# Kernel optimization log

Hardware: AMD Instinct MI355X
Metric: run time of the kernel (lower is better)

## Reference

```python
import jax, jax.numpy as jnp
from jax import lax
import numpy as np


def _gru_step(gi, h, Whh, bhh):
    # torch GRU cell: gates ordered (r, z, n); gi = x @ Wih.T + bih precomputed
    gh = h @ Whh.T + bhh
    ir, iz, inn = jnp.split(gi, 3, axis=-1)
    hr, hz, hn = jnp.split(gh, 3, axis=-1)
    r = jax.nn.sigmoid(ir + hr)
    z = jax.nn.sigmoid(iz + hz)
    n = jnp.tanh(inn + r * hn)
    return (1.0 - z) * n + z * h


def setup_inputs() -> dict:
    key = jax.random.key(0)
    ks = jax.random.split(key, 12)
    B, T, F, Wd, H, L = 64, 80, 4096, 6000, 512, 32
    s = 0.05  # weight init scale
    return {
        "x": jax.random.uniform(ks[0], (B, T, F), jnp.float32),  # nonneg CNN features -> full video lengths
        "y": jax.random.randint(ks[1], (L, B), 0, Wd),           # time-major caption token ids
        "Wih_v": jax.random.normal(ks[2], (3 * H, F), jnp.float32) * s,
        "Whh_v": jax.random.normal(ks[3], (3 * H, H), jnp.float32) * s,
        "bih_v": jax.random.normal(ks[4], (3 * H,), jnp.float32) * s,
        "bhh_v": jax.random.normal(ks[5], (3 * H,), jnp.float32) * s,
        "Wih_c": jax.random.normal(ks[6], (3 * H, H + Wd), jnp.float32) * s,
        "Whh_c": jax.random.normal(ks[7], (3 * H, H), jnp.float32) * s,
        "bih_c": jax.random.normal(ks[8], (3 * H,), jnp.float32) * s,
        "bhh_c": jax.random.normal(ks[9], (3 * H,), jnp.float32) * s,
        "Wout": jax.random.normal(ks[10], (Wd, H), jnp.float32) * s,
        "bout": jax.random.normal(ks[11], (Wd,), jnp.float32) * s,
    }


def reference(x, y, Wih_v, Whh_v, bih_v, bhh_v, Wih_c, Whh_c, bih_c, bhh_c, Wout, bout):
    B, T, F = x.shape
    L = y.shape[0]
    H = Whh_v.shape[1]
    Wd = Wout.shape[0]
    dt = x.dtype

    # ---- encode stage: video GRU over full-length sequences (time-major) ----
    xs = jnp.transpose(x, (1, 0, 2))                       # [T,B,F]
    gi_v = jnp.einsum('tbf,gf->tbg', xs, Wih_v) + bih_v    # precompute input gates
    h0 = jnp.zeros((B, H), dt)

    def enc_v(h, gi):
        h2 = _gru_step(gi, h, Whh_v, bhh_v)
        return h2, h2

    _, enc_out = lax.scan(enc_v, h0, gi_v)                 # [T,B,H]

    # caption GRU over [enc_out ; zeros(word_dim)]; zero word part contributes nothing
    Wih_c_h = Wih_c[:, :H]                                 # [3H,H]
    Wih_c_w = Wih_c[:, H:]                                 # [3H,Wd]
    gi_c = jnp.einsum('tbh,gh->tbg', enc_out, Wih_c_h) + bih_c

    def enc_c(h, gi):
        h2 = _gru_step(gi, h, Whh_c, bhh_c)
        return h2, None

    # NOTE: original code assigns this final hidden to `hidden_video` (quirk preserved)
    hidden_video, _ = lax.scan(enc_c, h0, gi_c)            # [B,H]

    # ---- decode stage: steps i = 1 .. L-1, zero frame input, teacher forcing ----
    gi_zero = jnp.broadcast_to(bih_v, (B, 3 * H))          # x=0 -> input gates are just bias
    WcwT = Wih_c_w.T                                       # [Wd,3H]; one-hot matmul == row gather

    def dec(h_v, y_prev):
        h_v2 = _gru_step(gi_zero, h_v, Whh_v, bhh_v)
        gi = h_v2 @ Wih_c_h.T + WcwT[y_prev] + bih_c       # concat([out, one_hot(y_prev)]) @ Wih_c.T
        h_c = _gru_step(gi, h_v2, Whh_c, bhh_c)            # initial hidden = fresh video hidden (original quirk)
        logits = h_c @ Wout.T + bout
        return h_v2, logits

    _, logits = lax.scan(dec, hidden_video, y[:-1])        # [L-1,B,Wd]

    probs = jnp.zeros((B, L, Wd), dt)
    probs = probs.at[0, 0, 1].set(1.0)                     # probs[0,:,1]=1 survives only at t=0
    probs = probs.at[:, 1:].set(jnp.transpose(logits, (1, 0, 2)))

    # loss is overwritten each iteration in the original -> last step only (cross-entropy)
    logp = jax.nn.log_softmax(logits[-1], axis=-1)         # [B,Wd]
    loss = -jnp.take_along_axis(logp, y[-1][:, None], axis=1).mean()
    return probs, loss
```

## Files before the change

kernel.cpp:

```cpp
#include <hip/hip_runtime.h>

typedef short s16x8 __attribute__((ext_vector_type(8)));
typedef float f32x4 __attribute__((ext_vector_type(4)));
typedef unsigned short u16x4 __attribute__((ext_vector_type(4)));

#define MFMA_B16(a, b, c) __builtin_amdgcn_mfma_f32_16x16x32_bf16((a), (b), (c), 0, 0, 0)

__device__ __forceinline__ unsigned short f2b(float f) {
    unsigned u = __builtin_bit_cast(unsigned, f);
    u = (u + 0x7fffu + ((u >> 16) & 1u)) >> 16;
    return (unsigned short)u;
}
__device__ __forceinline__ float b2f(unsigned short h) {
    unsigned u = ((unsigned)h) << 16;
    return __builtin_bit_cast(float, u);
}
__device__ __forceinline__ float sigm(float x) { return 1.f / (1.f + __expf(-x)); }
__device__ __forceinline__ float tanh_f(float x) {
    float t = __expf(-2.f * fabsf(x));
    float r = (1.f - t) / (1.f + t);
    return copysignf(r, x);
}

__device__ __forceinline__ void stg_b16_sc(unsigned short* p, unsigned short v) {
    unsigned v32 = v;
    asm volatile("global_store_short %0, %1, off sc1" :: "v"(p), "v"(v32) : "memory");
}
__device__ __forceinline__ void stg_b32_sc(float* p, float v) {
    asm volatile("global_store_dword %0, %1, off sc1" :: "v"(p), "v"(v) : "memory");
}
__device__ __forceinline__ unsigned long long ldg_u64_sc(const void* p) {
    return __hip_atomic_load((unsigned long long*)p, __ATOMIC_RELAXED, __HIP_MEMORY_SCOPE_AGENT);
}
__device__ __forceinline__ float ldg_b16_sc(const unsigned short* p) {
    unsigned short v = __hip_atomic_load((unsigned short*)p, __ATOMIC_RELAXED, __HIP_MEMORY_SCOPE_AGENT);
    return b2f(v);
}
__device__ __forceinline__ float ldg_f32_sc(const float* p) {
    return __hip_atomic_load((float*)p, __ATOMIC_RELAXED, __HIP_MEMORY_SCOPE_AGENT);
}
__device__ __forceinline__ s16x8 ldA_sc(const unsigned short* p) {
    union { unsigned long long u[2]; s16x8 v; } r;
    r.u[0] = ldg_u64_sc(p);
    r.u[1] = ldg_u64_sc((const unsigned long long*)p + 1);
    return r.v;
}

__device__ __forceinline__ void block_publish(int* flag, int v) {
    asm volatile("s_waitcnt vmcnt(0)" ::: "memory");
    __syncthreads();
    if (threadIdx.x == 0)
        __hip_atomic_store(flag, v, __ATOMIC_RELAXED, __HIP_MEMORY_SCOPE_AGENT);
}
template <int SLP>
__device__ __forceinline__ void flags_wait2(const int* f1, int t1, const int* f2, int t2) {
    const int lane = threadIdx.x & 63;
    const int* ptr = (lane < 32) ? (f1 + lane * 16) : (f2 + (lane - 32) * 16);
    const int tgt = (lane < 32) ? t1 : t2;
    for (;;) {
        int v = __hip_atomic_load((int*)ptr, __ATOMIC_RELAXED, __HIP_MEMORY_SCOPE_AGENT);
        if (__all(v >= tgt)) break;
        __builtin_amdgcn_s_sleep(SLP);
    }
}
template <int SLP>
__device__ __forceinline__ void flags_wait(const int* f, int t) {
    flags_wait2<SLP>(f, t, f, t);
}
template <int SLP>
__device__ __forceinline__ void scalar_wait(int* c, int target) {
    while (__hip_atomic_load(c, __ATOMIC_RELAXED, __HIP_MEMORY_SCOPE_AGENT) < target)
        __builtin_amdgcn_s_sleep(SLP);
}
__device__ __forceinline__ void wave_add(int* c) {
    asm volatile("s_waitcnt vmcnt(0)" ::: "memory");
    if ((threadIdx.x & 63) == 0)
        __hip_atomic_fetch_add(c, 1, __ATOMIC_RELAXED, __HIP_MEMORY_SCOPE_AGENT);
}

#define WTILE 8192
#define WF(Wl, t, c, lane) (*(const s16x8*)((Wl) + (((t) * 16 + (c)) * 64 + (lane)) * 8))

__device__ __forceinline__ void stage_swz(const unsigned short* __restrict__ src,
                                          unsigned short* dst) {
    for (int idx = threadIdx.x; idx < 1024; idx += 256) {
        const int ln = idx & 63;
        *(uint4*)(dst + (size_t)idx * 8) =
            *(const uint4*)(src + (size_t)(ln & 15) * 512 + (ln >> 4) * 8 + ((idx >> 6)) * 32);
    }
}

__device__ __forceinline__ void mm3_s(const unsigned short* __restrict__ A, int m0,
                                      const unsigned short* Wl, int lane,
                                      f32x4& a0, f32x4& a1, f32x4& a2) {
    const unsigned short* ab = A + (size_t)(m0 + (lane & 15)) * 512 + (lane >> 4) * 8;
#pragma unroll
    for (int c = 0; c < 16; ++c) {
        s16x8 a = ldA_sc(ab + c * 32);
        a0 = MFMA_B16(a, WF(Wl, 0, c, lane), a0);
        a1 = MFMA_B16(a, WF(Wl, 1, c, lane), a1);
        a2 = MFMA_B16(a, WF(Wl, 2, c, lane), a2);
    }
}
__device__ __forceinline__ void mm6_s(const unsigned short* __restrict__ A0,
                                      const unsigned short* __restrict__ A1, int m0,
                                      const unsigned short* Wl, int lane,
                                      f32x4& aR, f32x4& aZ, f32x4& aIN, f32x4& aHN) {
    const unsigned short* a0 = A0 + (size_t)(m0 + (lane & 15)) * 512 + (lane >> 4) * 8;
    const unsigned short* a1 = A1 + (size_t)(m0 + (lane & 15)) * 512 + (lane >> 4) * 8;
#pragma unroll
    for (int c = 0; c < 16; ++c) {
        s16x8 x0 = ldA_sc(a0 + c * 32);
        s16x8 x1 = ldA_sc(a1 + c * 32);
        aR  = MFMA_B16(x0, WF(Wl, 0, c, lane), aR);
        aZ  = MFMA_B16(x0, WF(Wl, 1, c, lane), aZ);
        aIN = MFMA_B16(x0, WF(Wl, 2, c, lane), aIN);
        aR  = MFMA_B16(x1, WF(Wl, 3, c, lane), aR);
        aZ  = MFMA_B16(x1, WF(Wl, 4, c, lane), aZ);
        aHN = MFMA_B16(x1, WF(Wl, 5, c, lane), aHN);
    }
}

__global__ void prep_kernel(const float* __restrict__ x, const float* __restrict__ Wih_v,
                            const float* __restrict__ Whh_v, const float* __restrict__ Whh_c,
                            const float* __restrict__ Wih_c, const float* __restrict__ Wout,
                            unsigned short* __restrict__ xB, unsigned short* __restrict__ WihB,
                            unsigned short* __restrict__ WhhvB, unsigned short* __restrict__ WhhcB,
                            unsigned short* __restrict__ WchhB, unsigned short* __restrict__ WoutB,
                            unsigned short* __restrict__ zeroB, int* __restrict__ ctrs,
                            float* __restrict__ out) {
    const int n = gridDim.x * blockDim.x;
    const int id0 = blockIdx.x * blockDim.x + threadIdx.x;
    for (int i = id0; i < 5242880; i += n) {
        const int e = i * 4;
        const int f = e & 4095, bt = e >> 12;
        const int b = bt / 80, t = bt - b * 80;
        float4 v = *(const float4*)(x + (size_t)e);
        u16x4 s = {f2b(v.x), f2b(v.y), f2b(v.z), f2b(v.w)};
        *(u16x4*)(xB + (size_t)(t * 64 + b) * 4096 + f) = s;
    }
    for (int i = id0; i < 1572864; i += n) {
        float4 v = *(const float4*)(Wih_v + (size_t)i * 4);
        u16x4 s = {f2b(v.x), f2b(v.y), f2b(v.z), f2b(v.w)};
        *(u16x4*)(WihB + (size_t)i * 4) = s;
    }
    for (int i = id0; i < 786432; i += n) {
        WhhvB[i] = f2b(Whh_v[i]);
        WhhcB[i] = f2b(Whh_c[i]);
        WchhB[i] = f2b(Wih_c[(size_t)(i >> 9) * 6512 + (i & 511)]);
    }
    for (int i = id0; i < 3072000; i += n) WoutB[i] = f2b(Wout[i]);
    for (int i = id0; i < 384000; i += n)
        out[(size_t)(i / 6000) * 192000 + (i % 6000)] = (i == 1) ? 1.f : 0.f;
    for (int i = id0; i < 32768; i += n) zeroB[i] = 0;
    for (int i = id0; i < 4096; i += n) ctrs[i] = 0;
}

__global__ __launch_bounds__(256) void gemm1_kernel(const unsigned short* __restrict__ xB,
                                                    const unsigned short* __restrict__ WihB,
                                                    const float* __restrict__ bih,
                                                    float* __restrict__ gi) {
    __shared__ unsigned short As[128 * 40];
    __shared__ unsigned short Bs[128 * 40];
    const int bm = blockIdx.x % 40;
    const int bn = blockIdx.x / 40;
    const int m0 = bm * 128, n0 = bn * 128;
    const int tid = threadIdx.x;
    const int lane = tid & 63;
    const int wave = tid >> 6;
    const int wm = (wave >> 1) * 64, wn = (wave & 1) * 64;
    const int quad = lane >> 4, l15 = lane & 15;

    const f32x4 z4 = {0.f, 0.f, 0.f, 0.f};
    f32x4 acc[4][4];
#pragma unroll
    for (int i = 0; i < 4; ++i)
#pragma unroll
        for (int j = 0; j < 4; ++j) acc[i][j] = z4;

    const int sr = tid >> 1;
    const int sc0 = (tid & 1) * 16;

    for (int k0 = 0; k0 < 4096; k0 += 32) {
        __syncthreads();
#pragma unroll
        for (int p = 0; p < 2; ++p) {
            const int c8 = sc0 + p * 8;
            *(s16x8*)&As[sr * 40 + c8] =
                *(const s16x8*)(xB + (size_t)(m0 + sr) * 4096 + k0 + c8);
            *(s16x8*)&Bs[sr * 40 + c8] =
                *(const s16x8*)(WihB + (size_t)(n0 + sr) * 4096 + k0 + c8);
        }
        __syncthreads();
        s16x8 af[4], bfr[4];
#pragma unroll
        for (int i = 0; i < 4; ++i) af[i] = *(const s16x8*)&As[(wm + i * 16 + l15) * 40 + quad * 8];
#pragma unroll
        for (int j = 0; j < 4; ++j) bfr[j] = *(const s16x8*)&Bs[(wn + j * 16 + l15) * 40 + quad * 8];
#pragma unroll
        for (int i = 0; i < 4; ++i)
#pragma unroll
            for (int j = 0; j < 4; ++j) acc[i][j] = MFMA_B16(af[i], bfr[j], acc[i][j]);
    }
#pragma unroll
    for (int i = 0; i < 4; ++i)
#pragma unroll
        for (int j = 0; j < 4; ++j)
#pragma unroll
            for (int r = 0; r < 4; ++r) {
                const int m = m0 + wm + i * 16 + quad * 4 + r;
                const int nn = n0 + wn + j * 16 + l15;
                gi[(size_t)m * 1536 + nn] = acc[i][j][r] + bih[nn];
            }
}

struct SeqParams {
    const float* bih_v; const float* bhh_v;
    const float* bih_c; const float* bhh_c;
    const float* bout;  const int* y;
    const float* gi;    const float* Wc;  float* out;
    const unsigned short* WhhvB; const unsigned short* WhhcB; const unsigned short* WchhB;
    const unsigned short* WoutB; unsigned short* WcwTB;
    unsigned short* eo;
    unsigned short* hv2B;
    float*          hv2F;
    unsigned short* hcdB;
    unsigned short* ecb0; unsigned short* ecb1; unsigned short* zeroB;
    float* hcf; float* lossP; int* ctr;
};
#define F_EO (p.ctr)
#define F_EC (p.ctr + 512)
#define F_HV (p.ctr + 1024)
#define F_HC (p.ctr + 1536)
#define S_TR (p.ctr + 2048)
#define S_LOG (p.ctr + 2064)
#define S_LP (p.ctr + 2080)

__global__ __launch_bounds__(256, 1) void seq_kernel(SeqParams p) {
    __shared__ unsigned short Wlds[49152];
    const int blk = blockIdx.x;
    const int lane = threadIdx.x & 63;
    const int wave = threadIdx.x >> 6;
    const int quad = lane >> 4, l15 = lane & 15;
    const f32x4 z4 = {0.f, 0.f, 0.f, 0.f};

    if (blk < 32) {
        const int j0 = blk * 16;
        const int j = j0 + l15;
        const int m0 = wave * 16;
        const int b_ = m0 + quad * 4;
#pragma unroll
        for (int g = 0; g < 3; ++g)
            stage_swz(p.WhhvB + (size_t)(g * 512 + j0) * 512, Wlds + g * WTILE);
        __syncthreads();
        const float bhr = p.bhh_v[j], bhz = p.bhh_v[512 + j], bhn = p.bhh_v[1024 + j];
        float hp[4] = {0.f, 0.f, 0.f, 0.f};

        for (int t = 0; t < 80; ++t) {
            float gr[4], gz[4], gn[4];
            const float* gt = p.gi + (size_t)t * 98304;
#pragma unroll
            for (int r = 0; r < 4; ++r) {
                const float* gb = gt + (size_t)(b_ + r) * 1536;
                gr[r] = gb[j]; gz[r] = gb[512 + j]; gn[r] = gb[1024 + j];
            }
            f32x4 aR = z4, aZ = z4, aN = z4;
            if (t > 0) {
                flags_wait<1>(F_EO, t);
                mm3_s(p.eo + (size_t)(t - 1) * 32768, m0, Wlds, lane, aR, aZ, aN);
            }
            unsigned short* eoW = p.eo + (size_t)t * 32768;
#pragma unroll
            for (int r = 0; r < 4; ++r) {
                float rg = sigm(gr[r] + aR[r] + bhr);
                float zg = sigm(gz[r] + aZ[r] + bhz);
                float ng = tanh_f(gn[r] + rg * (aN[r] + bhn));
                float hn = (1.f - zg) * ng + zg * hp[r];
                hp[r] = hn;
                stg_b16_sc(eoW + (size_t)(b_ + r) * 512 + j, f2b(hn));
            }
            block_publish(F_EO + blk * 16, t + 1);
        }

        flags_wait<1>(F_EC, 80);
        const float bir = p.bih_v[j], biz = p.bih_v[512 + j], bin_ = p.bih_v[1024 + j];
        for (int s = 0; s <= 30; ++s) {
            if (s > 0) flags_wait<1>(F_HV, s);
            f32x4 aR = z4, aZ = z4, aN = z4;
            mm3_s(p.hv2B + (size_t)s * 32768, m0, Wlds, lane, aR, aZ, aN);
            unsigned short* hw = p.hv2B + (size_t)(s + 1) * 32768;
            float* hwF = p.hv2F + (size_t)(s + 1) * 32768;
#pragma unroll
            for (int r = 0; r < 4; ++r) {
                float hpv = (s == 0) ? ldg_f32_sc(p.hcf + (size_t)(b_ + r) * 512 + j) : hp[r];
                float rg = sigm(bir + aR[r] + bhr);
                float zg = sigm(biz + aZ[r] + bhz);
                float ng = tanh_f(bin_ + rg * (aN[r] + bhn));
                float hn = (1.f - zg) * ng + zg * hpv;
                hp[r] = hn;
                stg_b16_sc(hw + (size_t)(b_ + r) * 512 + j, f2b(hn));
                stg_b32_sc(hwF + (size_t)(b_ + r) * 512 + j, hn);
            }
            block_publish(F_HV + blk * 16, s + 1);
        }

        if (blk < 16) {
            const int b = (blk << 2) | wave;
            scalar_wait<2>(S_LOG, 125);
            const float* lg = p.out + (size_t)b * 192000 + 186000;
            float m = -1e30f, sum = 0.f;
            for (int i = lane; i < 3000; i += 64) {
                union { unsigned long long u; float f[2]; } pr;
                pr.u = ldg_u64_sc(lg + 2 * i);
#pragma unroll
                for (int e = 0; e < 2; ++e) {
                    float v = pr.f[e];
                    float nm = fmaxf(m, v);
                    sum = sum * __expf(m - nm) + __expf(v - nm);
                    m = nm;
                }
            }
#pragma unroll
            for (int off = 32; off > 0; off >>= 1) {
                float m2 = __shfl_down(m, off);
                float s2 = __shfl_down(sum, off);
                float nm = fmaxf(m, m2);
                sum = sum * __expf(m - nm) + s2 * __expf(m2 - nm);
                m = nm;
            }
            if (lane == 0) {
                int yv = p.y[31 * 64 + b];
                float lgy = ldg_f32_sc(lg + yv);
                stg_b32_sc(p.lossP + b, (m + __logf(sum)) - lgy);
            }
            wave_add(S_LP);
            if (blk == 0 && wave == 0) {
                scalar_wait<1>(S_LP, 64);
                float v = ldg_f32_sc(p.lossP + lane);
#pragma unroll
                for (int off = 32; off > 0; off >>= 1) v += __shfl_down(v, off);
                if (lane == 0) p.out[12288000] = v * (1.f / 64.f);
            }
        }
    } else if (blk < 64) {
        const int cid = blk - 32;
        const int j0 = cid * 16;
        const int j = j0 + l15;
        const int m0 = wave * 16;
        const int b_ = m0 + quad * 4;
#pragma unroll
        for (int g = 0; g < 3; ++g) {
            stage_swz(p.WchhB + (size_t)(g * 512 + j0) * 512, Wlds + g * WTILE);
            stage_swz(p.WhhcB + (size_t)(g * 512 + j0) * 512, Wlds + (3 + g) * WTILE);
        }
        __syncthreads();
        const float bcr = p.bih_c[j] + p.bhh_c[j];
        const float bcz = p.bih_c[512 + j] + p.bhh_c[512 + j];
        const float bin_ = p.bih_c[1024 + j];
        const float bhn = p.bhh_c[1024 + j];
        float hp[4] = {0.f, 0.f, 0.f, 0.f};

        for (int t = 0; t < 80; ++t) {
            flags_wait2<1>(F_EO, t + 1, F_EC, t);
            const unsigned short* A1 = (t == 0) ? p.zeroB : ((t & 1) ? p.ecb0 : p.ecb1);
            unsigned short* ew = (t & 1) ? p.ecb1 : p.ecb0;
            f32x4 aR = z4, aZ = z4, aIN = z4, aHN = z4;
            mm6_s(p.eo + (size_t)t * 32768, A1, m0, Wlds, lane, aR, aZ, aIN, aHN);
#pragma unroll
            for (int r = 0; r < 4; ++r) {
                float rg = sigm(aR[r] + bcr);
                float zg = sigm(aZ[r] + bcz);
                float ng = tanh_f(aIN[r] + bin_ + rg * (aHN[r] + bhn));
                float hn = (1.f - zg) * ng + zg * hp[r];
                hp[r] = hn;
                unsigned short hb = f2b(hn);
                stg_b16_sc(ew + (size_t)(b_ + r) * 512 + j, hb);
                if (t == 79) {
                    stg_b16_sc(p.hv2B + (size_t)(b_ + r) * 512 + j, hb);
                    stg_b32_sc(p.hcf + (size_t)(b_ + r) * 512 + j, hn);
                }
            }
            block_publish(F_EC + cid * 16, t + 1);
        }

        scalar_wait<4>(S_TR, 94);
        for (int s = 0; s <= 30; ++s) {
            float er[4], ez[4], en[4];
#pragma unroll
            for (int r = 0; r < 4; ++r) {
                const int yv = p.y[s * 64 + (b_ + r)];
                const unsigned short* em = p.WcwTB + (size_t)yv * 1536;
                er[r] = ldg_b16_sc(em + j);
                ez[r] = ldg_b16_sc(em + 512 + j);
                en[r] = ldg_b16_sc(em + 1024 + j);
            }
            flags_wait<1>(F_HV, s + 1);
            const unsigned short* hv = p.hv2B + (size_t)(s + 1) * 32768;
            const float* hvF = p.hv2F + (size_t)(s + 1) * 32768;
            f32x4 aR = z4, aZ = z4, aIN = z4, aHN = z4;
            mm6_s(hv, hv, m0, Wlds, lane, aR, aZ, aIN, aHN);
            unsigned short* hc = p.hcdB + (size_t)s * 32768;
#pragma unroll
            for (int r = 0; r < 4; ++r) {
                float rg = sigm(aR[r] + er[r] + bcr);
                float zg = sigm(aZ[r] + ez[r] + bcz);
                float ng = tanh_f(aIN[r] + en[r] + bin_ + rg * (aHN[r] + bhn));
                float hpv = ldg_f32_sc(hvF + (size_t)(b_ + r) * 512 + j);
                stg_b16_sc(hc + (size_t)(b_ + r) * 512 + j, f2b((1.f - zg) * ng + zg * hpv));
            }
            block_publish(F_HC + cid * 16, s + 1);
        }
    } else {
        const int bo = blk - 64;
        const int w0 = bo * 48;
#pragma unroll
        for (int tl = 0; tl < 3; ++tl)
            stage_swz(p.WoutB + (size_t)(w0 + tl * 16) * 512, Wlds + tl * WTILE);
        __syncthreads();

        if (bo < 94) {
            float* tile = (float*)(Wlds + 24576);
            const int w0t = bo * 64;
            const int tx = threadIdx.x & 63, ty = threadIdx.x >> 6;
            for (int gt = 0; gt < 24; ++gt) {
                const int g0 = gt * 64;
                __syncthreads();
                for (int r = ty; r < 64; r += 4) {
                    int w = w0t + tx;
                    tile[r * 65 + tx] = (w < 6000) ? p.Wc[(size_t)(g0 + r) * 6512 + 512 + w] : 0.f;
                }
                __syncthreads();
                for (int r = ty; r < 64; r += 4) {
                    int w = w0t + r;
                    if (w < 6000)
                        stg_b16_sc(p.WcwTB + (size_t)w * 1536 + g0 + tx, f2b(tile[tx * 65 + r]));
                }
            }
            asm volatile("s_waitcnt vmcnt(0)" ::: "memory");
            __syncthreads();
            if (threadIdx.x == 0)
                __hip_atomic_fetch_add(S_TR, 1, __ATOMIC_RELAXED, __HIP_MEMORY_SCOPE_AGENT);
        }

        const int m0 = wave * 16;
        const int b_ = m0 + quad * 4;
        float bo_[3];
#pragma unroll
        for (int tl = 0; tl < 3; ++tl) bo_[tl] = p.bout[w0 + tl * 16 + l15];

        for (int s = 0; s <= 30; ++s) {
            flags_wait<2>(F_HC, s + 1);
            const unsigned short* ab =
                p.hcdB + (size_t)s * 32768 + (size_t)(m0 + l15) * 512 + quad * 8;
            s16x8 af[16];
#pragma unroll
            for (int c = 0; c < 16; ++c) af[c] = ldA_sc(ab + c * 32);
#pragma unroll
            for (int tl = 0; tl < 3; ++tl) {
                f32x4 acc = z4;
#pragma unroll
                for (int c = 0; c < 16; ++c) acc = MFMA_B16(af[c], WF(Wlds, tl, c, lane), acc);
#pragma unroll
                for (int r = 0; r < 4; ++r)
                    stg_b32_sc(p.out + (size_t)(b_ + r) * 192000 + (size_t)(s + 1) * 6000 +
                                   w0 + tl * 16 + l15,
                               acc[r] + bo_[tl]);
            }
        }
        asm volatile("s_waitcnt vmcnt(0)" ::: "memory");
        __syncthreads();
        if (threadIdx.x == 0)
            __hip_atomic_fetch_add(S_LOG, 1, __ATOMIC_RELAXED, __HIP_MEMORY_SCOPE_AGENT);
    }
}

extern "C" void kernel_launch(void* const* d_in, const int* in_sizes, int n_in,
                              void* d_out, int out_size, void* d_ws, size_t ws_size,
                              hipStream_t stream) {
    const float* x     = (const float*)d_in[0];
    const int*   y     = (const int*)d_in[1];
    const float* Wih_v = (const float*)d_in[2];
    const float* Whh_v = (const float*)d_in[3];
    const float* bih_v = (const float*)d_in[4];
    const float* bhh_v = (const float*)d_in[5];
    const float* Wih_c = (const float*)d_in[6];
    const float* Whh_c = (const float*)d_in[7];
    const float* bih_c = (const float*)d_in[8];
    const float* bhh_c = (const float*)d_in[9];
    const float* Wout  = (const float*)d_in[10];
    const float* bout  = (const float*)d_in[11];
    float* out = (float*)d_out;

    char* w = (char*)d_ws;
    size_t o = 0;
    auto alloc = [&](size_t bytes) -> void* {
        void* p = (void*)(w + o);
        o += (bytes + 255) & ~(size_t)255;
        return p;
    };
    float*          gi    = (float*)alloc(7864320ull * 4);
    unsigned short* xB    = (unsigned short*)alloc(20971520ull * 2);
    unsigned short* WihB  = (unsigned short*)alloc(6291456ull * 2);
    unsigned short* WhhvB = (unsigned short*)alloc(786432ull * 2);
    unsigned short* WhhcB = (unsigned short*)alloc(786432ull * 2);
    unsigned short* WchhB = (unsigned short*)alloc(786432ull * 2);
    unsigned short* WoutB = (unsigned short*)alloc(3072000ull * 2);
    unsigned short* WcwTB = (unsigned short*)alloc(9216000ull * 2);
    unsigned short* eo    = (unsigned short*)alloc(80ull * 32768 * 2);
    unsigned short* hv2B  = (unsigned short*)alloc(32ull * 32768 * 2);
    float*          hv2F  = (float*)alloc(32ull * 32768 * 4);
    unsigned short* hcdB  = (unsigned short*)alloc(31ull * 32768 * 2);
    unsigned short* ecb0  = (unsigned short*)alloc(32768ull * 2);
    unsigned short* ecb1  = (unsigned short*)alloc(32768ull * 2);
    unsigned short* zeroB = (unsigned short*)alloc(32768ull * 2);
    float*          hcf   = (float*)alloc(32768ull * 4);
    float*          lossP = (float*)alloc(64ull * 4);
    int*            ctrs  = (int*)alloc(4096ull * 4);
    if (o > ws_size) return;

    prep_kernel<<<512, 256, 0, stream>>>(x, Wih_v, Whh_v, Whh_c, Wih_c, Wout, xB, WihB,
                                         WhhvB, WhhcB, WchhB, WoutB, zeroB, ctrs, out);
    gemm1_kernel<<<480, 256, 0, stream>>>(xB, WihB, bih_v, gi);

    SeqParams p;
    p.bih_v = bih_v; p.bhh_v = bhh_v; p.bih_c = bih_c; p.bhh_c = bhh_c;
    p.bout = bout; p.y = y; p.gi = gi; p.Wc = Wih_c; p.out = out;
    p.WhhvB = WhhvB; p.WhhcB = WhhcB; p.WchhB = WchhB; p.WoutB = WoutB; p.WcwTB = WcwTB;
    p.eo = eo; p.hv2B = hv2B; p.hv2F = hv2F; p.hcdB = hcdB;
    p.ecb0 = ecb0; p.ecb1 = ecb1; p.zeroB = zeroB;
    p.hcf = hcf; p.lossP = lossP; p.ctr = ctrs;
    void* args[] = {&p};
    hipLaunchCooperativeKernel((void*)seq_kernel, dim3(189), dim3(256), args, 0, stream);
}
```

Before: 1.430 ms.

## Assign persistent-kernel roles by XCD and use XCD-local L2 paths for recurrence

The cooperative sequence kernel now reads each block's XCC ID at startup and assigns roles so that the video-GRU blocks share one XCD and the caption-GRU blocks share another. Those blocks exchange hidden states through XCD-local buffers and flags using plain or sc0 loads, which keeps the traffic in the local L2 instead of going through device-scope coherent accesses. If the per-XCD slot counts do not come out as expected, role assignment falls back to block index, and flag waits that time out switch to the remote coherent path. The change also widens the grid to 256 blocks with 2-tile output workers, keeps the full caption-state history instead of a double buffer, and vectorises the weight conversion in prep. This relies on undocumented cross-XCD cache behaviour and adds duplicate stores.

```diff
diff --git a/kernel.cpp b/kernel.cpp
--- a/kernel.cpp
+++ b/kernel.cpp
@@ -46,11 +46,25 @@
     return r.v;
 }
 
+__device__ __forceinline__ int ld_flag_sc0(const int* p) {
+    int v;
+    asm volatile("global_load_dword %0, %1, off sc0\n\ts_waitcnt vmcnt(0)"
+                 : "=v"(v) : "v"(p) : "memory");
+    return v;
+}
+
+#define TMO 3000
+
 __device__ __forceinline__ void block_publish(int* flag, int v) {
     asm volatile("s_waitcnt vmcnt(0)" ::: "memory");
     __syncthreads();
     if (threadIdx.x == 0)
         __hip_atomic_store(flag, v, __ATOMIC_RELAXED, __HIP_MEMORY_SCOPE_AGENT);
+}
+__device__ __forceinline__ void publish_l(int* fl, int v) {
+    asm volatile("s_waitcnt vmcnt(0)" ::: "memory");
+    __syncthreads();
+    if (threadIdx.x == 0) *(volatile int*)fl = v;
 }
 template <int SLP>
 __device__ __forceinline__ void flags_wait2(const int* f1, int t1, const int* f2, int t2) {
@@ -68,6 +82,40 @@
     flags_wait2<SLP>(f, t, f, t);
 }
 template <int SLP>
+__device__ __forceinline__ void wait32(const int* fl, const int* fr, int t, int& fb) {
+    const int li = threadIdx.x & 31;
+    int it = 0;
+    for (;;) {
+        int v;
+        if (!fb) v = ld_flag_sc0(fl + li);
+        else v = __hip_atomic_load((int*)(fr + li * 16), __ATOMIC_RELAXED, __HIP_MEMORY_SCOPE_AGENT);
+        if (__all(v >= t)) return;
+        if (!fb && ++it > TMO) fb = 1;
+        __builtin_amdgcn_s_sleep(SLP);
+    }
+}
+template <int SLP>
+__device__ __forceinline__ void wait_rl(const int* fr1, int t1, const int* fl2, const int* fr2,
+                                        int t2, int& fb) {
+    const int lane = threadIdx.x & 63;
+    int it = 0;
+    for (;;) {
+        int v, tg;
+        if (lane < 32) {
+            v = __hip_atomic_load((int*)(fr1 + lane * 16), __ATOMIC_RELAXED, __HIP_MEMORY_SCOPE_AGENT);
+            tg = t1;
+        } else {
+            const int li = lane - 32;
+            if (!fb) v = ld_flag_sc0(fl2 + li);
+            else v = __hip_atomic_load((int*)(fr2 + li * 16), __ATOMIC_RELAXED, __HIP_MEMORY_SCOPE_AGENT);
+            tg = t2;
+        }
+        if (__all(v >= tg)) return;
+        if (!fb && ++it > TMO) fb = 1;
+        __builtin_amdgcn_s_sleep(SLP);
+    }
+}
+template <int SLP>
 __device__ __forceinline__ void scalar_wait(int* c, int target) {
     while (__hip_atomic_load(c, __ATOMIC_RELAXED, __HIP_MEMORY_SCOPE_AGENT) < target)
         __builtin_amdgcn_s_sleep(SLP);
@@ -102,6 +150,18 @@
         a2 = MFMA_B16(a, WF(Wl, 2, c, lane), a2);
     }
 }
+__device__ __forceinline__ void mm3_p(const unsigned short* __restrict__ A, int m0,
+                                      const unsigned short* Wl, int lane,
+                                      f32x4& a0, f32x4& a1, f32x4& a2) {
+    const unsigned short* ab = A + (size_t)(m0 + (lane & 15)) * 512 + (lane >> 4) * 8;
+#pragma unroll
+    for (int c = 0; c < 16; ++c) {
+        s16x8 a = *(const s16x8*)(ab + c * 32);
+        a0 = MFMA_B16(a, WF(Wl, 0, c, lane), a0);
+        a1 = MFMA_B16(a, WF(Wl, 1, c, lane), a1);
+        a2 = MFMA_B16(a, WF(Wl, 2, c, lane), a2);
+    }
+}
 __device__ __forceinline__ void mm6_s(const unsigned short* __restrict__ A0,
                                       const unsigned short* __restrict__ A1, int m0,
                                       const unsigned short* Wl, int lane,
@@ -112,6 +172,24 @@
     for (int c = 0; c < 16; ++c) {
         s16x8 x0 = ldA_sc(a0 + c * 32);
         s16x8 x1 = ldA_sc(a1 + c * 32);
+        aR  = MFMA_B16(x0, WF(Wl, 0, c, lane), aR);
+        aZ  = MFMA_B16(x0, WF(Wl, 1, c, lane), aZ);
+        aIN = MFMA_B16(x0, WF(Wl, 2, c, lane), aIN);
+        aR  = MFMA_B16(x1, WF(Wl, 3, c, lane), aR);
+        aZ  = MFMA_B16(x1, WF(Wl, 4, c, lane), aZ);
+        aHN = MFMA_B16(x1, WF(Wl, 5, c, lane), aHN);
+    }
+}
+__device__ __forceinline__ void mm6_rp(const unsigned short* __restrict__ A0,
+                                       const unsigned short* __restrict__ A1, int m0,
+                                       const unsigned short* Wl, int lane,
+                                       f32x4& aR, f32x4& aZ, f32x4& aIN, f32x4& aHN) {
+    const unsigned short* a0 = A0 + (size_t)(m0 + (lane & 15)) * 512 + (lane >> 4) * 8;
+    const unsigned short* a1 = A1 + (size_t)(m0 + (lane & 15)) * 512 + (lane >> 4) * 8;
+#pragma unroll
+    for (int c = 0; c < 16; ++c) {
+        s16x8 x0 = ldA_sc(a0 + c * 32);
+        s16x8 x1 = *(const s16x8*)(a1 + c * 32);
         aR  = MFMA_B16(x0, WF(Wl, 0, c, lane), aR);
         aZ  = MFMA_B16(x0, WF(Wl, 1, c, lane), aZ);
         aIN = MFMA_B16(x0, WF(Wl, 2, c, lane), aIN);
@@ -144,15 +222,26 @@
         u16x4 s = {f2b(v.x), f2b(v.y), f2b(v.z), f2b(v.w)};
         *(u16x4*)(WihB + (size_t)i * 4) = s;
     }
-    for (int i = id0; i < 786432; i += n) {
-        WhhvB[i] = f2b(Whh_v[i]);
-        WhhcB[i] = f2b(Whh_c[i]);
-        WchhB[i] = f2b(Wih_c[(size_t)(i >> 9) * 6512 + (i & 511)]);
-    }
-    for (int i = id0; i < 3072000; i += n) WoutB[i] = f2b(Wout[i]);
+    for (int i = id0; i < 196608; i += n) {
+        const int e = i * 4;
+        float4 a = *(const float4*)(Whh_v + e);
+        u16x4 sa = {f2b(a.x), f2b(a.y), f2b(a.z), f2b(a.w)};
+        *(u16x4*)(WhhvB + e) = sa;
+        float4 b = *(const float4*)(Whh_c + e);
+        u16x4 sb = {f2b(b.x), f2b(b.y), f2b(b.z), f2b(b.w)};
+        *(u16x4*)(WhhcB + e) = sb;
+        float4 d = *(const float4*)(Wih_c + (size_t)(e >> 9) * 6512 + (e & 511));
+        u16x4 sd = {f2b(d.x), f2b(d.y), f2b(d.z), f2b(d.w)};
+        *(u16x4*)(WchhB + e) = sd;
+    }
+    for (int i = id0; i < 768000; i += n) {
+        float4 a = *(const float4*)(Wout + (size_t)i * 4);
+        u16x4 s = {f2b(a.x), f2b(a.y), f2b(a.z), f2b(a.w)};
+        *(u16x4*)(WoutB + (size_t)i * 4) = s;
+    }
     for (int i = id0; i < 384000; i += n)
         out[(size_t)(i / 6000) * 192000 + (i % 6000)] = (i == 1) ? 1.f : 0.f;
-    for (int i = id0; i < 32768; i += n) zeroB[i] = 0;
+    for (int i = id0; i < 8192; i += n) ((unsigned long long*)zeroB)[i] = 0ull;
     for (int i = id0; i < 4096; i += n) ctrs[i] = 0;
 }
 
@@ -222,255 +311,364 @@
     const unsigned short* WhhvB; const unsigned short* WhhcB; const unsigned short* WchhB;
     const unsigned short* WoutB; unsigned short* WcwTB;
     unsigned short* eo;
+    unsigned short* eoL;
     unsigned short* hv2B;
+    unsigned short* hv2L;
     float*          hv2F;
     unsigned short* hcdB;
-    unsigned short* ecb0; unsigned short* ecb1; unsigned short* zeroB;
+    unsigned short* ecA;
+    unsigned short* zeroB;
     float* hcf; float* lossP; int* ctr;
 };
-#define F_EO (p.ctr)
-#define F_EC (p.ctr + 512)
-#define F_HV (p.ctr + 1024)
-#define F_HC (p.ctr + 1536)
-#define S_TR (p.ctr + 2048)
+#define F_EOr (p.ctr)
+#define F_ECr (p.ctr + 512)
+#define F_HVr (p.ctr + 1024)
+#define F_HCr (p.ctr + 1536)
+#define S_TR  (p.ctr + 2048)
 #define S_LOG (p.ctr + 2064)
-#define S_LP (p.ctr + 2080)
-
-__global__ __launch_bounds__(256, 1) void seq_kernel(SeqParams p) {
-    __shared__ unsigned short Wlds[49152];
-    const int blk = blockIdx.x;
+#define S_LP  (p.ctr + 2080)
+#define F_EOl (p.ctr + 2304)
+#define F_ECl (p.ctr + 2336)
+#define F_HVl (p.ctr + 2368)
+#define R_XCNT (p.ctr + 2432)
+#define R_TOT  (p.ctr + 2448)
+
+template <bool L>
+__device__ __forceinline__ void run_v(const SeqParams& p, int vid, unsigned short* Wlds) {
     const int lane = threadIdx.x & 63;
     const int wave = threadIdx.x >> 6;
     const int quad = lane >> 4, l15 = lane & 15;
     const f32x4 z4 = {0.f, 0.f, 0.f, 0.f};
-
-    if (blk < 32) {
-        const int j0 = blk * 16;
-        const int j = j0 + l15;
-        const int m0 = wave * 16;
-        const int b_ = m0 + quad * 4;
-#pragma unroll
-        for (int g = 0; g < 3; ++g)
-            stage_swz(p.WhhvB + (size_t)(g * 512 + j0) * 512, Wlds + g * WTILE);
-        __syncthreads();
-        const float bhr = p.bhh_v[j], bhz = p.bhh_v[512 + j], bhn = p.bhh_v[1024 + j];
-        float hp[4] = {0.f, 0.f, 0.f, 0.f};
-
-        for (int t = 0; t < 80; ++t) {
-            float gr[4], gz[4], gn[4];
-            const float* gt = p.gi + (size_t)t * 98304;
-#pragma unroll
-            for (int r = 0; r < 4; ++r) {
-                const float* gb = gt + (size_t)(b_ + r) * 1536;
-                gr[r] = gb[j]; gz[r] = gb[512 + j]; gn[r] = gb[1024 + j];
-            }
-            f32x4 aR = z4, aZ = z4, aN = z4;
-            if (t > 0) {
-                flags_wait<1>(F_EO, t);
+    const int j0 = vid * 16;
+    const int j = j0 + l15;
+    const int m0 = wave * 16;
+    const int b_ = m0 + quad * 4;
+#pragma unroll
+    for (int g = 0; g < 3; ++g)
+        stage_swz(p.WhhvB + (size_t)(g * 512 + j0) * 512, Wlds + g * WTILE);
+    __syncthreads();
+    const float bhr = p.bhh_v[j], bhz = p.bhh_v[512 + j], bhn = p.bhh_v[1024 + j];
+    float hp[4] = {0.f, 0.f, 0.f, 0.f};
+    int fbv = 0;
+
+    for (int t = 0; t < 80; ++t) {
+        float gr[4], gz[4], gn[4];
+        const float* gt = p.gi + (size_t)t * 98304;
+#pragma unroll
+        for (int r = 0; r < 4; ++r) {
+            const float* gb = gt + (size_t)(b_ + r) * 1536;
+            gr[r] = gb[j]; gz[r] = gb[512 + j]; gn[r] = gb[1024 + j];
+        }
+        f32x4 aR = z4, aZ = z4, aN = z4;
+        if (t > 0) {
+            if (L) {
+                wait32<1>(F_EOl, F_EOr, t, fbv);
+                mm3_p(p.eoL + (size_t)(t - 1) * 32768, m0, Wlds, lane, aR, aZ, aN);
+            } else {
+                flags_wait<1>(F_EOr, t);
                 mm3_s(p.eo + (size_t)(t - 1) * 32768, m0, Wlds, lane, aR, aZ, aN);
             }
-            unsigned short* eoW = p.eo + (size_t)t * 32768;
-#pragma unroll
-            for (int r = 0; r < 4; ++r) {
-                float rg = sigm(gr[r] + aR[r] + bhr);
-                float zg = sigm(gz[r] + aZ[r] + bhz);
-                float ng = tanh_f(gn[r] + rg * (aN[r] + bhn));
-                float hn = (1.f - zg) * ng + zg * hp[r];
-                hp[r] = hn;
-                stg_b16_sc(eoW + (size_t)(b_ + r) * 512 + j, f2b(hn));
+        }
+        unsigned short hb[4];
+#pragma unroll
+        for (int r = 0; r < 4; ++r) {
+            float rg = sigm(gr[r] + aR[r] + bhr);
+            float zg = sigm(gz[r] + aZ[r] + bhz);
+            float ng = tanh_f(gn[r] + rg * (aN[r] + bhn));
+            float hn = (1.f - zg) * ng + zg * hp[r];
+            hp[r] = hn;
+            hb[r] = f2b(hn);
+        }
+        if (L) {
+            unsigned short* el = p.eoL + (size_t)t * 32768;
+#pragma unroll
+            for (int r = 0; r < 4; ++r) el[(size_t)(b_ + r) * 512 + j] = hb[r];
+            publish_l(F_EOl + vid, t + 1);
+        }
+        unsigned short* er = p.eo + (size_t)t * 32768;
+#pragma unroll
+        for (int r = 0; r < 4; ++r) stg_b16_sc(er + (size_t)(b_ + r) * 512 + j, hb[r]);
+        block_publish(F_EOr + vid * 16, t + 1);
+    }
+
+    flags_wait<1>(F_ECr, 80);
+    const float bir = p.bih_v[j], biz = p.bih_v[512 + j], bin_ = p.bih_v[1024 + j];
+    for (int s = 0; s <= 30; ++s) {
+        if (s > 0) {
+            if (L) wait32<1>(F_HVl, F_HVr, s, fbv);
+            else   flags_wait<1>(F_HVr, s);
+        }
+        f32x4 aR = z4, aZ = z4, aN = z4;
+        if (s == 0)      mm3_s(p.hv2B, m0, Wlds, lane, aR, aZ, aN);
+        else if (L)      mm3_p(p.hv2L + (size_t)s * 32768, m0, Wlds, lane, aR, aZ, aN);
+        else             mm3_s(p.hv2B + (size_t)s * 32768, m0, Wlds, lane, aR, aZ, aN);
+        float hn4[4];
+#pragma unroll
+        for (int r = 0; r < 4; ++r) {
+            float hpv = (s == 0) ? ldg_f32_sc(p.hcf + (size_t)(b_ + r) * 512 + j) : hp[r];
+            float rg = sigm(bir + aR[r] + bhr);
+            float zg = sigm(biz + aZ[r] + bhz);
+            float ng = tanh_f(bin_ + rg * (aN[r] + bhn));
+            float hn = (1.f - zg) * ng + zg * hpv;
+            hp[r] = hn;
+            hn4[r] = hn;
+        }
+        if (L) {
+            unsigned short* hl = p.hv2L + (size_t)(s + 1) * 32768;
+#pragma unroll
+            for (int r = 0; r < 4; ++r) hl[(size_t)(b_ + r) * 512 + j] = f2b(hn4[r]);
+            publish_l(F_HVl + vid, s + 1);
+        }
+        unsigned short* hw = p.hv2B + (size_t)(s + 1) * 32768;
+        float* hwF = p.hv2F + (size_t)(s + 1) * 32768;
+#pragma unroll
+        for (int r = 0; r < 4; ++r) {
+            stg_b16_sc(hw + (size_t)(b_ + r) * 512 + j, f2b(hn4[r]));
+            stg_b32_sc(hwF + (size_t)(b_ + r) * 512 + j, hn4[r]);
+        }
+        block_publish(F_HVr + vid * 16, s + 1);
+    }
+
+    if (vid < 16) {
+        const int b = (vid << 2) | wave;
+        scalar_wait<2>(S_LOG, 188);
+        const float* lg = p.out + (size_t)b * 192000 + 186000;
+        float m = -1e30f, sum = 0.f;
+        for (int i = lane; i < 3000; i += 64) {
+            union { unsigned long long u; float f[2]; } pr;
+            pr.u = ldg_u64_sc(lg + 2 * i);
+#pragma unroll
+            for (int e = 0; e < 2; ++e) {
+                float v = pr.f[e];
+                float nm = fmaxf(m, v);
+                sum = sum * __expf(m - nm) + __expf(v - nm);
+                m = nm;
             }
-            block_publish(F_EO + blk * 16, t + 1);
-        }
-
-        flags_wait<1>(F_EC, 80);
-        const float bir = p.bih_v[j], biz = p.bih_v[512 + j], bin_ = p.bih_v[1024 + j];
-        for (int s = 0; s <= 30; ++s) {
-            if (s > 0) flags_wait<1>(F_HV, s);
-            f32x4 aR = z4, aZ = z4, aN = z4;
-            mm3_s(p.hv2B + (size_t)s * 32768, m0, Wlds, lane, aR, aZ, aN);
-            unsigned short* hw = p.hv2B + (size_t)(s + 1) * 32768;
-            float* hwF = p.hv2F + (size_t)(s + 1) * 32768;
-#pragma unroll
-            for (int r = 0; r < 4; ++r) {
-                float hpv = (s == 0) ? ldg_f32_sc(p.hcf + (size_t)(b_ + r) * 512 + j) : hp[r];
-                float rg = sigm(bir + aR[r] + bhr);
-                float zg = sigm(biz + aZ[r] + bhz);
-                float ng = tanh_f(bin_ + rg * (aN[r] + bhn));
-                float hn = (1.f - zg) * ng + zg * hpv;
-                hp[r] = hn;
-                stg_b16_sc(hw + (size_t)(b_ + r) * 512 + j, f2b(hn));
-                stg_b32_sc(hwF + (size_t)(b_ + r) * 512 + j, hn);
-            }
-            block_publish(F_HV + blk * 16, s + 1);
-        }
-
-        if (blk < 16) {
-            const int b = (blk << 2) | wave;
-            scalar_wait<2>(S_LOG, 125);
-            const float* lg = p.out + (size_t)b * 192000 + 186000;
-            float m = -1e30f, sum = 0.f;
-            for (int i = lane; i < 3000; i += 64) {
-                union { unsigned long long u; float f[2]; } pr;
-                pr.u = ldg_u64_sc(lg + 2 * i);
-#pragma unroll
-                for (int e = 0; e < 2; ++e) {
-                    float v = pr.f[e];
-                    float nm = fmaxf(m, v);
-                    sum = sum * __expf(m - nm) + __expf(v - nm);
-                    m = nm;
+        }
+#pragma unroll
+        for (int off = 32; off > 0; off >>= 1) {
+            float m2 = __shfl_down(m, off);
+            float s2 = __shfl_down(sum, off);
+            float nm = fmaxf(m, m2);
+            sum = sum * __expf(m - nm) + s2 * __expf(m2 - nm);
+            m = nm;
+        }
+        if (lane == 0) {
+            int yv = p.y[31 * 64 + b];
+            float lgy = ldg_f32_sc(lg + yv);
+            stg_b32_sc(p.lossP + b, (m + __logf(sum)) - lgy);
+        }
+        wave_add(S_LP);
+        if (vid == 0 && wave == 0) {
+            scalar_wait<1>(S_LP, 64);
+            float v = ldg_f32_sc(p.lossP + lane);
+#pragma unroll
+            for (int off = 32; off > 0; off >>= 1) v += __shfl_down(v, off);
+            if (lane == 0) p.out[12288000] = v * (1.f / 64.f);
+        }
+    }
+}
+
+template <bool L>
+__device__ __forceinline__ void run_c(const SeqParams& p, int cid, unsigned short* Wlds) {
+    const int lane = threadIdx.x & 63;
+    const int wave = threadIdx.x >> 6;
+    const int quad = lane >> 4, l15 = lane & 15;
+    const f32x4 z4 = {0.f, 0.f, 0.f, 0.f};
+    const int j0 = cid * 16;
+    const int j = j0 + l15;
+    const int m0 = wave * 16;
+    const int b_ = m0 + quad * 4;
+#pragma unroll
+    for (int g = 0; g < 3; ++g) {
+        stage_swz(p.WchhB + (size_t)(g * 512 + j0) * 512, Wlds + g * WTILE);
+        stage_swz(p.WhhcB + (size_t)(g * 512 + j0) * 512, Wlds + (3 + g) * WTILE);
+    }
+    __syncthreads();
+    const float bcr = p.bih_c[j] + p.bhh_c[j];
+    const float bcz = p.bih_c[512 + j] + p.bhh_c[512 + j];
+    const float bin_ = p.bih_c[1024 + j];
+    const float bhn = p.bhh_c[1024 + j];
+    float hp[4] = {0.f, 0.f, 0.f, 0.f};
+    int fbc = 0;
+
+    for (int t = 0; t < 80; ++t) {
+        if (L) wait_rl<1>(F_EOr, t + 1, F_ECl, F_ECr, t, fbc);
+        else   flags_wait2<1>(F_EOr, t + 1, F_ECr, t);
+        const unsigned short* A1 = (t == 0) ? p.zeroB : p.ecA + (size_t)(t - 1) * 32768;
+        f32x4 aR = z4, aZ = z4, aIN = z4, aHN = z4;
+        if (L) mm6_rp(p.eo + (size_t)t * 32768, A1, m0, Wlds, lane, aR, aZ, aIN, aHN);
+        else   mm6_s (p.eo + (size_t)t * 32768, A1, m0, Wlds, lane, aR, aZ, aIN, aHN);
+        unsigned short hb[4]; float hn4[4];
+#pragma unroll
+        for (int r = 0; r < 4; ++r) {
+            float rg = sigm(aR[r] + bcr);
+            float zg = sigm(aZ[r] + bcz);
+            float ng = tanh_f(aIN[r] + bin_ + rg * (aHN[r] + bhn));
+            float hn = (1.f - zg) * ng + zg * hp[r];
+            hp[r] = hn;
+            hn4[r] = hn;
+            hb[r] = f2b(hn);
+        }
+        unsigned short* ew = p.ecA + (size_t)t * 32768;
+        if (L) {
+#pragma unroll
+            for (int r = 0; r < 4; ++r) ew[(size_t)(b_ + r) * 512 + j] = hb[r];
+            publish_l(F_ECl + cid, t + 1);
+            if (t == 79) {
+#pragma unroll
+                for (int r = 0; r < 4; ++r) {
+                    stg_b16_sc(p.hv2B + (size_t)(b_ + r) * 512 + j, hb[r]);
+                    stg_b32_sc(p.hcf + (size_t)(b_ + r) * 512 + j, hn4[r]);
                 }
             }
-#pragma unroll
-            for (int off = 32; off > 0; off >>= 1) {
-                float m2 = __shfl_down(m, off);
-                float s2 = __shfl_down(sum, off);
-                float nm = fmaxf(m, m2);
-                sum = sum * __expf(m - nm) + s2 * __expf(m2 - nm);
-                m = nm;
-            }
-            if (lane == 0) {
-                int yv = p.y[31 * 64 + b];
-                float lgy = ldg_f32_sc(lg + yv);
-                stg_b32_sc(p.lossP + b, (m + __logf(sum)) - lgy);
-            }
-            wave_add(S_LP);
-            if (blk == 0 && wave == 0) {
-                scalar_wait<1>(S_LP, 64);
-                float v = ldg_f32_sc(p.lossP + lane);
-#pragma unroll
-                for (int off = 32; off > 0; off >>= 1) v += __shfl_down(v, off);
-                if (lane == 0) p.out[12288000] = v * (1.f / 64.f);
-            }
-        }
-    } else if (blk < 64) {
-        const int cid = blk - 32;
-        const int j0 = cid * 16;
-        const int j = j0 + l15;
-        const int m0 = wave * 16;
-        const int b_ = m0 + quad * 4;
-#pragma unroll
-        for (int g = 0; g < 3; ++g) {
-            stage_swz(p.WchhB + (size_t)(g * 512 + j0) * 512, Wlds + g * WTILE);
-            stage_swz(p.WhhcB + (size_t)(g * 512 + j0) * 512, Wlds + (3 + g) * WTILE);
-        }
-        __syncthreads();
-        const float bcr = p.bih_c[j] + p.bhh_c[j];
-        const float bcz = p.bih_c[512 + j] + p.bhh_c[512 + j];
-        const float bin_ = p.bih_c[1024 + j];
-        const float bhn = p.bhh_c[1024 + j];
-        float hp[4] = {0.f, 0.f, 0.f, 0.f};
-
-        for (int t = 0; t < 80; ++t) {
-            flags_wait2<1>(F_EO, t + 1, F_EC, t);
-            const unsigned short* A1 = (t == 0) ? p.zeroB : ((t & 1) ? p.ecb0 : p.ecb1);
-            unsigned short* ew = (t & 1) ? p.ecb1 : p.ecb0;
-            f32x4 aR = z4, aZ = z4, aIN = z4, aHN = z4;
-            mm6_s(p.eo + (size_t)t * 32768, A1, m0, Wlds, lane, aR, aZ, aIN, aHN);
+            block_publish(F_ECr + cid * 16, t + 1);
+        } else {
 #pragma unroll
             for (int r = 0; r < 4; ++r) {
-                float rg = sigm(aR[r] + bcr);
-                float zg = sigm(aZ[r] + bcz);
-                float ng = tanh_f(aIN[r] + bin_ + rg * (aHN[r] + bhn));
-                float hn = (1.f - zg) * ng + zg * hp[r];
-                hp[r] = hn;
-                unsigned short hb = f2b(hn);
-                stg_b16_sc(ew + (size_t)(b_ + r) * 512 + j, hb);
+                stg_b16_sc(ew + (size_t)(b_ + r) * 512 + j, hb[r]);
                 if (t == 79) {
-                    stg_b16_sc(p.hv2B + (size_t)(b_ + r) * 512 + j, hb);
-                    stg_b32_sc(p.hcf + (size_t)(b_ + r) * 512 + j, hn);
+                    stg_b16_sc(p.hv2B + (size_t)(b_ + r) * 512 + j, hb[r]);
+                    stg_b32_sc(p.hcf + (size_t)(b_ + r) * 512 + j, hn4[r]);
                 }
             }
-            block_publish(F_EC + cid * 16, t + 1);
-        }
-
-        scalar_wait<4>(S_TR, 94);
-        for (int s = 0; s <= 30; ++s) {
-            float er[4], ez[4], en[4];
-#pragma unroll
-            for (int r = 0; r < 4; ++r) {
-                const int yv = p.y[s * 64 + (b_ + r)];
-                const unsigned short* em = p.WcwTB + (size_t)yv * 1536;
-                er[r] = ldg_b16_sc(em + j);
-                ez[r] = ldg_b16_sc(em + 512 + j);
-                en[r] = ldg_b16_sc(em + 1024 + j);
+            block_publish(F_ECr + cid * 16, t + 1);
+        }
+    }
+
+    scalar_wait<4>(S_TR, 94);
+    for (int s = 0; s <= 30; ++s) {
+        float er[4], ez[4], en[4];
+#pragma unroll
+        for (int r = 0; r < 4; ++r) {
+            const int yv = p.y[s * 64 + (b_ + r)];
+            const unsigned short* em = p.WcwTB + (size_t)yv * 1536;
+            er[r] = ldg_b16_sc(em + j);
+            ez[r] = ldg_b16_sc(em + 512 + j);
+            en[r] = ldg_b16_sc(em + 1024 + j);
+        }
+        flags_wait<1>(F_HVr, s + 1);
+        const unsigned short* hv = p.hv2B + (size_t)(s + 1) * 32768;
+        const float* hvF = p.hv2F + (size_t)(s + 1) * 32768;
+        f32x4 aR = z4, aZ = z4, aIN = z4, aHN = z4;
+        mm6_s(hv, hv, m0, Wlds, lane, aR, aZ, aIN, aHN);
+        unsigned short* hc = p.hcdB + (size_t)s * 32768;
+#pragma unroll
+        for (int r = 0; r < 4; ++r) {
+            float rg = sigm(aR[r] + er[r] + bcr);
+            float zg = sigm(aZ[r] + ez[r] + bcz);
+            float ng = tanh_f(aIN[r] + en[r] + bin_ + rg * (aHN[r] + bhn));
+            float hpv = ldg_f32_sc(hvF + (size_t)(b_ + r) * 512 + j);
+            stg_b16_sc(hc + (size_t)(b_ + r) * 512 + j, f2b((1.f - zg) * ng + zg * hpv));
+        }
+        block_publish(F_HCr + cid * 16, s + 1);
+    }
+}
+
+__device__ __forceinline__ void run_o(const SeqParams& p, int oid, unsigned short* Wlds) {
+    if (oid >= 188) return;
+    const int lane = threadIdx.x & 63;
+    const int wave = threadIdx.x >> 6;
+    const int quad = lane >> 4, l15 = lane & 15;
+    const f32x4 z4 = {0.f, 0.f, 0.f, 0.f};
+    const int w0 = oid * 32;
+    const int ntl = (w0 + 32 <= 6000) ? 2 : 1;
+    for (int tl = 0; tl < ntl; ++tl)
+        stage_swz(p.WoutB + (size_t)(w0 + tl * 16) * 512, Wlds + tl * WTILE);
+    __syncthreads();
+
+    if (oid < 94) {
+        float* tile = (float*)(Wlds + 16384);
+        const int w0t = oid * 64;
+        const int tx = threadIdx.x & 63, ty = threadIdx.x >> 6;
+        for (int gt = 0; gt < 24; ++gt) {
+            const int g0 = gt * 64;
+            __syncthreads();
+            for (int r = ty; r < 64; r += 4) {
+                int w = w0t + tx;
+                tile[r * 65 + tx] = (w < 6000) ? p.Wc[(size_t)(g0 + r) * 6512 + 512 + w] : 0.f;
             }
-            flags_wait<1>(F_HV, s + 1);
-            const unsigned short* hv = p.hv2B + (size_t)(s + 1) * 32768;
-            const float* hvF = p.hv2F + (size_t)(s + 1) * 32768;
-            f32x4 aR = z4, aZ = z4, aIN = z4, aHN = z4;
-            mm6_s(hv, hv, m0, Wlds, lane, aR, aZ, aIN, aHN);
-            unsigned short* hc = p.hcdB + (size_t)s * 32768;
-#pragma unroll
-            for (int r = 0; r < 4; ++r) {
-                float rg = sigm(aR[r] + er[r] + bcr);
-                float zg = sigm(aZ[r] + ez[r] + bcz);
-                float ng = tanh_f(aIN[r] + en[r] + bin_ + rg * (aHN[r] + bhn));
-                float hpv = ldg_f32_sc(hvF + (size_t)(b_ + r) * 512 + j);
-                stg_b16_sc(hc + (size_t)(b_ + r) * 512 + j, f2b((1.f - zg) * ng + zg * hpv));
-            }
-            block_publish(F_HC + cid * 16, s + 1);
-        }
-    } else {
-        const int bo = blk - 64;
-        const int w0 = bo * 48;
-#pragma unroll
-        for (int tl = 0; tl < 3; ++tl)
-            stage_swz(p.WoutB + (size_t)(w0 + tl * 16) * 512, Wlds + tl * WTILE);
-        __syncthreads();
-
-        if (bo < 94) {
-            float* tile = (float*)(Wlds + 24576);
-            const int w0t = bo * 64;
-            const int tx = threadIdx.x & 63, ty = threadIdx.x >> 6;
-            for (int gt = 0; gt < 24; ++gt) {
-                const int g0 = gt * 64;
-                __syncthreads();
-                for (int r = ty; r < 64; r += 4) {
-                    int w = w0t + tx;
-                    tile[r * 65 + tx] = (w < 6000) ? p.Wc[(size_t)(g0 + r) * 6512 + 512 + w] : 0.f;
-                }
-                __syncthreads();
-                for (int r = ty; r < 64; r += 4) {
-                    int w = w0t + r;
-                    if (w < 6000)
-                        stg_b16_sc(p.WcwTB + (size_t)w * 1536 + g0 + tx, f2b(tile[tx * 65 + r]));
-                }
-            }
-            asm volatile("s_waitcnt vmcnt(0)" ::: "memory");
             __syncthreads();
-            if (threadIdx.x == 0)
-                __hip_atomic_fetch_add(S_TR, 1, __ATOMIC_RELAXED, __HIP_MEMORY_SCOPE_AGENT);
-        }
-
-        const int m0 = wave * 16;
-        const int b_ = m0 + quad * 4;
-        float bo_[3];
-#pragma unroll
-        for (int tl = 0; tl < 3; ++tl) bo_[tl] = p.bout[w0 + tl * 16 + l15];
-
-        for (int s = 0; s <= 30; ++s) {
-            flags_wait<2>(F_HC, s + 1);
-            const unsigned short* ab =
-                p.hcdB + (size_t)s * 32768 + (size_t)(m0 + l15) * 512 + quad * 8;
-            s16x8 af[16];
-#pragma unroll
-            for (int c = 0; c < 16; ++c) af[c] = ldA_sc(ab + c * 32);
-#pragma unroll
-            for (int tl = 0; tl < 3; ++tl) {
-                f32x4 acc = z4;
-#pragma unroll
-                for (int c = 0; c < 16; ++c) acc = MFMA_B16(af[c], WF(Wlds, tl, c, lane), acc);
-#pragma unroll
-                for (int r = 0; r < 4; ++r)
-                    stg_b32_sc(p.out + (size_t)(b_ + r) * 192000 + (size_t)(s + 1) * 6000 +
-                                   w0 + tl * 16 + l15,
-                               acc[r] + bo_[tl]);
+            for (int r = ty; r < 64; r += 4) {
+                int w = w0t + r;
+                if (w < 6000)
+                    stg_b16_sc(p.WcwTB + (size_t)w * 1536 + g0 + tx, f2b(tile[tx * 65 + r]));
             }
         }
         asm volatile("s_waitcnt vmcnt(0)" ::: "memory");
         __syncthreads();
         if (threadIdx.x == 0)
-            __hip_atomic_fetch_add(S_LOG, 1, __ATOMIC_RELAXED, __HIP_MEMORY_SCOPE_AGENT);
+            __hip_atomic_fetch_add(S_TR, 1, __ATOMIC_RELAXED, __HIP_MEMORY_SCOPE_AGENT);
+    }
+
+    const int m0 = wave * 16;
+    const int b_ = m0 + quad * 4;
+    float bo_[2];
+#pragma unroll
+    for (int tl = 0; tl < 2; ++tl) {
+        int bi = w0 + tl * 16 + l15;
+        bo_[tl] = p.bout[bi < 6000 ? bi : 5999];
+    }
+    for (int s = 0; s <= 30; ++s) {
+        if (wave == 0) flags_wait<2>(F_HCr, s + 1);
+        __syncthreads();
+        const unsigned short* ab =
+            p.hcdB + (size_t)s * 32768 + (size_t)(m0 + l15) * 512 + quad * 8;
+        s16x8 af[16];
+#pragma unroll
+        for (int c = 0; c < 16; ++c) af[c] = ldA_sc(ab + c * 32);
+        for (int tl = 0; tl < ntl; ++tl) {
+            f32x4 acc = z4;
+#pragma unroll
+            for (int c = 0; c < 16; ++c) acc = MFMA_B16(af[c], WF(Wlds, tl, c, lane), acc);
+#pragma unroll
+            for (int r = 0; r < 4; ++r)
+                stg_b32_sc(p.out + (size_t)(b_ + r) * 192000 + (size_t)(s + 1) * 6000 +
+                               w0 + tl * 16 + l15,
+                           acc[r] + bo_[tl]);
+        }
+    }
+    asm volatile("s_waitcnt vmcnt(0)" ::: "memory");
+    __syncthreads();
+    if (threadIdx.x == 0)
+        __hip_atomic_fetch_add(S_LOG, 1, __ATOMIC_RELAXED, __HIP_MEMORY_SCOPE_AGENT);
+}
+
+__global__ __launch_bounds__(256, 1) void seq_kernel(SeqParams p) {
+    __shared__ unsigned short Wlds[49152];
+    __shared__ int s_role[3];
+    if (threadIdx.x == 0) {
+        int xcd;
+        asm volatile("s_getreg_b32 %0, hwreg(HW_REG_XCC_ID)" : "=s"(xcd));
+        xcd &= 7;
+        int slot = __hip_atomic_fetch_add(R_XCNT + xcd, 1, __ATOMIC_RELAXED, __HIP_MEMORY_SCOPE_AGENT);
+        __hip_atomic_fetch_add(R_TOT, 1, __ATOMIC_RELAXED, __HIP_MEMORY_SCOPE_AGENT);
+        const int nb = (int)gridDim.x;
+        while (__hip_atomic_load(R_TOT, __ATOMIC_RELAXED, __HIP_MEMORY_SCOPE_AGENT) < nb)
+            __builtin_amdgcn_s_sleep(2);
+        int ok = 1;
+        for (int i = 0; i < 8; ++i)
+            ok &= (__hip_atomic_load(R_XCNT + i, __ATOMIC_RELAXED, __HIP_MEMORY_SCOPE_AGENT) == 32);
+        int role, idx;
+        if (ok) {
+            if (xcd == 0)      { role = 0; idx = slot; }
+            else if (xcd == 1) { role = 1; idx = slot; }
+            else               { role = 2; idx = slot + 32 * (xcd - 2); }
+        } else {
+            role = (blockIdx.x < 32) ? 0 : ((blockIdx.x < 64) ? 1 : 2);
+            idx = (role == 0) ? (int)blockIdx.x
+                              : ((role == 1) ? (int)blockIdx.x - 32 : (int)blockIdx.x - 64);
+        }
+        s_role[0] = role; s_role[1] = idx; s_role[2] = ok;
+    }
+    __syncthreads();
+    const int role = s_role[0], idx = s_role[1], loc = s_role[2];
+    if (role == 0) {
+        if (loc) run_v<true>(p, idx, Wlds); else run_v<false>(p, idx, Wlds);
+    } else if (role == 1) {
+        if (loc) run_c<true>(p, idx, Wlds); else run_c<false>(p, idx, Wlds);
+    } else {
+        run_o(p, idx, Wlds);
     }
 }
 
@@ -507,11 +705,12 @@
     unsigned short* WoutB = (unsigned short*)alloc(3072000ull * 2);
     unsigned short* WcwTB = (unsigned short*)alloc(9216000ull * 2);
     unsigned short* eo    = (unsigned short*)alloc(80ull * 32768 * 2);
+    unsigned short* eoL   = (unsigned short*)alloc(80ull * 32768 * 2);
     unsigned short* hv2B  = (unsigned short*)alloc(32ull * 32768 * 2);
+    unsigned short* hv2L  = (unsigned short*)alloc(32ull * 32768 * 2);
     float*          hv2F  = (float*)alloc(32ull * 32768 * 4);
     unsigned short* hcdB  = (unsigned short*)alloc(31ull * 32768 * 2);
-    unsigned short* ecb0  = (unsigned short*)alloc(32768ull * 2);
-    unsigned short* ecb1  = (unsigned short*)alloc(32768ull * 2);
+    unsigned short* ecA   = (unsigned short*)alloc(80ull * 32768 * 2);
     unsigned short* zeroB = (unsigned short*)alloc(32768ull * 2);
     float*          hcf   = (float*)alloc(32768ull * 4);
     float*          lossP = (float*)alloc(64ull * 4);
@@ -526,9 +725,9 @@
     p.bih_v = bih_v; p.bhh_v = bhh_v; p.bih_c = bih_c; p.bhh_c = bhh_c;
     p.bout = bout; p.y = y; p.gi = gi; p.Wc = Wih_c; p.out = out;
     p.WhhvB = WhhvB; p.WhhcB = WhhcB; p.WchhB = WchhB; p.WoutB = WoutB; p.WcwTB = WcwTB;
-    p.eo = eo; p.hv2B = hv2B; p.hv2F = hv2F; p.hcdB = hcdB;
-    p.ecb0 = ecb0; p.ecb1 = ecb1; p.zeroB = zeroB;
+    p.eo = eo; p.eoL = eoL; p.hv2B = hv2B; p.hv2L = hv2L; p.hv2F = hv2F; p.hcdB = hcdB;
+    p.ecA = ecA; p.zeroB = zeroB;
     p.hcf = hcf; p.lossP = lossP; p.ctr = ctrs;
     void* args[] = {&p};
-    hipLaunchCooperativeKernel((void*)seq_kernel, dim3(189), dim3(256), args, 0, stream);
-}
+    hipLaunchCooperativeKernel((void*)seq_kernel, dim3(256), dim3(256), args, 0, stream);
+}
```

After: 1.573 ms. 10.0% more time.
